# Optimization experiments

Hardware: AMD Instinct MI355X
Metric: run time of the kernel (lower is better)

Reference implementation:

```python
import jax, jax.numpy as jnp
import numpy as np
import math

B, S, DM, H = 2, 2048, 1024, 16
HD = DM // H  # head_dim = 64


def setup_inputs() -> dict:
    key = jax.random.key(0)
    ks = jax.random.split(key, 7)
    mk = lambda k, shp, s=1.0: jax.random.normal(k, shp, dtype=jnp.float32) * s
    return {
        "q": mk(ks[0], (B, S, DM)),
        "k": mk(ks[1], (B, S, DM)),
        "v": mk(ks[2], (B, S, DM)),
        "wq": mk(ks[3], (DM, DM), 0.02),
        "wk": mk(ks[4], (DM, DM), 0.02),
        "wv": mk(ks[5], (DM, DM), 0.02),
        "wo": mk(ks[6], (DM, DM), 0.02),
    }


def reference(q, k, v, wq, wk, wv, wo):
    bsz, seqlen, _ = q.shape
    # bias-free linear projections: y = x @ W.T (torch nn.Linear layout [out,in])
    def proj(x, w):
        y = jnp.einsum('bsd,ed->bse', x, w)
        return y.reshape(bsz, seqlen, H, HD).transpose(0, 2, 1, 3)  # (B,H,S,HD)
    xq, xk, xv = proj(q, wq), proj(k, wk), proj(v, wv)
    scores = jnp.einsum('bhqd,bhkd->bhqk', xq, xk) / math.sqrt(HD)  # (B,H,S,S)
    # causal mask: -inf above the diagonal
    causal = jnp.tril(jnp.ones((seqlen, seqlen), dtype=bool))
    scores = jnp.where(causal[None, None], scores, -jnp.inf)
    probs = jax.nn.softmax(scores.astype(jnp.float32), axis=-1).astype(xq.dtype)
    # dropout p=0.0 -> identity in eval / p=0 config
    out = jnp.einsum('bhqk,bhkd->bhqd', probs, xv)  # (B,H,S,HD)
    out = out.transpose(0, 2, 1, 3).reshape(bsz, seqlen, DM)
    return jnp.einsum('bsd,ed->bse', out, wo)
```

## Files before the change

### kernel.cpp

```cpp
#include <hip/hip_runtime.h>
#include <hip/hip_bf16.h>
#include <stdint.h>

#define NB 2
#define NS 2048
#define NDM 1024
#define NH 16
#define NHD 64
#define NTOK (NB * NS)

typedef __bf16 bf16x8 __attribute__((ext_vector_type(8)));
typedef float f32x4 __attribute__((ext_vector_type(4)));
typedef uint16_t u16x8 __attribute__((ext_vector_type(8)));

static __device__ __forceinline__ uint16_t f2bf(float f) {
  __bf16 b = (__bf16)f;
  union { __bf16 b; uint16_t u; } x; x.b = b;
  return x.u;
}

static __device__ __forceinline__ u16x8 cvt8(float4 a, float4 b) {
  u16x8 v;
  v[0] = f2bf(a.x); v[1] = f2bf(a.y); v[2] = f2bf(a.z); v[3] = f2bf(a.w);
  v[4] = f2bf(b.x); v[5] = f2bf(b.y); v[6] = f2bf(b.z); v[7] = f2bf(b.w);
  return v;
}

static __device__ __forceinline__ void gload_lds16(const void* g, void* l) {
  __builtin_amdgcn_global_load_lds(
      (const __attribute__((address_space(1))) void*)g,
      (__attribute__((address_space(3))) void*)l, 16, 0, 0);
}

__global__ __launch_bounds__(256) void cvt_all(
    const float* __restrict__ wq, const float* __restrict__ wk,
    const float* __restrict__ wv, const float* __restrict__ wo,
    const float* __restrict__ q, const float* __restrict__ k,
    const float* __restrict__ v, uint16_t* __restrict__ WQB,
    uint16_t* __restrict__ WKB, uint16_t* __restrict__ WVB,
    uint16_t* __restrict__ WOB, uint16_t* __restrict__ XBQ,
    uint16_t* __restrict__ XBK, uint16_t* __restrict__ XBV) {
  size_t E = ((size_t)blockIdx.x * 256 + threadIdx.x) * 8;
  const float* src;
  uint16_t* dst;
  size_t off;
  if (E < (size_t)(4u << 20)) {
    int s = (int)(E >> 20);
    off = E & ((1u << 20) - 1);
    src = (s == 0) ? wq : (s == 1) ? wk : (s == 2) ? wv : wo;
    dst = (s == 0) ? WQB : (s == 1) ? WKB : (s == 2) ? WVB : WOB;
  } else {
    size_t E2 = E - ((size_t)4u << 20);
    int s = (int)(E2 >> 22);
    off = E2 & ((1u << 22) - 1);
    src = (s == 0) ? q : (s == 1) ? k : v;
    dst = (s == 0) ? XBQ : (s == 1) ? XBK : XBV;
  }
  float4 a = *(const float4*)(src + off);
  float4 b = *(const float4*)(src + off + 4);
  *(u16x8*)&dst[off] = cvt8(a, b);
}

__global__ __launch_bounds__(256) void proj_gemm(
    const uint16_t* __restrict__ xbq, const uint16_t* __restrict__ xbk,
    const uint16_t* __restrict__ xbv, const uint16_t* __restrict__ wqb,
    const uint16_t* __restrict__ wkb, const uint16_t* __restrict__ wvb,
    uint16_t* __restrict__ XQ, uint16_t* __restrict__ XK,
    uint16_t* __restrict__ XVT) {
  __shared__ uint16_t SM[2][2][128][64];
  int z = blockIdx.z;
  const uint16_t* A = (z == 0) ? xbq : (z == 1) ? xbk : xbv;
  const uint16_t* W = (z == 0) ? wqb : (z == 1) ? wkb : wvb;
  int m0 = blockIdx.x * 128, n0 = blockIdx.y * 128;
  int tid = threadIdx.x;
  int lane = tid & 63, w = tid >> 6;
  int g = lane >> 4, r16 = lane & 15;
  int wm = w >> 1, wn = w & 1;
  int bce = ((lane & 7) ^ ((lane >> 3) & 7)) * 8;
  int brlane = lane >> 3;

  f32x4 acc[4][4] = {};

  #pragma unroll
  for (int i = 0; i < 4; ++i) {
    int row = w * 32 + i * 8;
    gload_lds16(A + (size_t)(m0 + row + brlane) * NDM + bce, &SM[0][0][row][0]);
    gload_lds16(W + (size_t)(n0 + row + brlane) * NDM + bce, &SM[0][1][row][0]);
  }
  __syncthreads();

  for (int t = 0; t < 16; ++t) {
    int cur = t & 1, nxt = cur ^ 1;
    if (t < 15) {
      int k1 = (t + 1) * 64;
      #pragma unroll
      for (int i = 0; i < 4; ++i) {
        int row = w * 32 + i * 8;
        gload_lds16(A + (size_t)(m0 + row + brlane) * NDM + k1 + bce,
                    &SM[nxt][0][row][0]);
        gload_lds16(W + (size_t)(n0 + row + brlane) * NDM + k1 + bce,
                    &SM[nxt][1][row][0]);
      }
    }

    #pragma unroll
    for (int kc = 0; kc < 2; ++kc) {
      bf16x8 af[4], bf[4];
      #pragma unroll
      for (int i = 0; i < 4; ++i) {
        int gran = (kc * 4 + g) ^ (r16 & 7);
        af[i] = *(const bf16x8*)&SM[cur][0][wm * 64 + i * 16 + r16][gran * 8];
        bf[i] = *(const bf16x8*)&SM[cur][1][wn * 64 + i * 16 + r16][gran * 8];
      }
      #pragma unroll
      for (int mi = 0; mi < 4; ++mi)
        #pragma unroll
        for (int ni = 0; ni < 4; ++ni)
          acc[mi][ni] = __builtin_amdgcn_mfma_f32_16x16x32_bf16(
              af[mi], bf[ni], acc[mi][ni], 0, 0, 0);
    }
    __syncthreads();
  }

  if (z == 2) {
    uint16_t* T = &SM[0][0][0][0];
    #pragma unroll
    for (int mi = 0; mi < 4; ++mi) {
      #pragma unroll
      for (int ni = 0; ni < 4; ++ni) {
        int tr = wn * 64 + ni * 16 + r16;
        int tc = wm * 64 + mi * 16 + g * 4;
        int gran = tc >> 3, sub = g & 1;
        f32x4 a = acc[mi][ni];
        ushort4 pk;
        pk.x = f2bf(a[0]); pk.y = f2bf(a[1]);
        pk.z = f2bf(a[2]); pk.w = f2bf(a[3]);
        *(ushort4*)(T + tr * 128 + ((gran ^ (tr & 7)) << 3) + (sub << 2)) = pk;
      }
    }
    __syncthreads();
    #pragma unroll
    for (int it = 0; it < 8; ++it) {
      int row = it * 16 + (tid >> 4);
      int grn = tid & 15;
      u16x8 vv = *(const u16x8*)(T + row * 128 + ((grn ^ (row & 7)) << 3));
      *(u16x8*)&XVT[(size_t)(n0 + row) * NTOK + m0 + grn * 8] = vv;
    }
  } else {
    float scale = (z == 0) ? 0.125f * 1.44269504088896340736f : 1.0f;
    uint16_t* Y = (z == 0) ? XQ : XK;
    #pragma unroll
    for (int mi = 0; mi < 4; ++mi) {
      #pragma unroll
      for (int ni = 0; ni < 4; ++ni) {
        int m = m0 + wm * 64 + mi * 16 + g * 4;
        int n = n0 + wn * 64 + ni * 16 + r16;
        f32x4 a = acc[mi][ni];
        #pragma unroll
        for (int j = 0; j < 4; ++j)
          Y[(size_t)(m + j) * NDM + n] = f2bf(a[j] * scale);
      }
    }
  }
}

__global__ __launch_bounds__(256) void attn_kernel(
    const uint16_t* __restrict__ XQ, const uint16_t* __restrict__ XK,
    const uint16_t* __restrict__ XVT, uint16_t* __restrict__ AO) {
  __shared__ uint16_t Klds[2][64][72];
  __shared__ uint16_t Vlds[2][64][72];
  __shared__ uint16_t Plds[4][16][72];

  int tid = threadIdx.x;
  int lane = tid & 63;
  int w = tid >> 6;
  int g = lane >> 4, r16 = lane & 15;
  int srow = tid >> 2;
  int scol = (tid & 3) * 16;

  int item = (int)blockIdx.x;
  int qc = 31 - (item >> 5);
  int bh = item & 31;
  int b = bh >> 4, h = bh & 15;
  int q0 = qc * 64;
  int q0w = q0 + w * 16;
  int T = qc + 1;

  const uint16_t* qb =
      XQ + (size_t)(b * NS + q0w + r16) * NDM + h * NHD + g * 8;
  bf16x8 qf0 = *(const bf16x8*)qb;
  bf16x8 qf1 = *(const bf16x8*)(qb + 32);

  f32x4 oacc[4] = {};
  float mrow = -1e30f, lsum = 0.f;

  const uint16_t* kbase = XK + (size_t)(b * NS + srow) * NDM + h * NHD + scol;
  const uint16_t* vbase = XVT + (size_t)(h * NHD + srow) * NTOK + b * NS + scol;

  u16x8 kr0 = *(const u16x8*)(kbase);
  u16x8 kr1 = *(const u16x8*)(kbase + 8);
  u16x8 vr0 = *(const u16x8*)(vbase);
  u16x8 vr1 = *(const u16x8*)(vbase + 8);

  for (int t = 0; t < T; ++t) {
    int kv0 = t * 64;
    int cur = t & 1;
    *(u16x8*)&Klds[cur][srow][scol]     = kr0;
    *(u16x8*)&Klds[cur][srow][scol + 8] = kr1;
    *(u16x8*)&Vlds[cur][srow][scol]     = vr0;
    *(u16x8*)&Vlds[cur][srow][scol + 8] = vr1;
    __syncthreads();
    if (t + 1 < T) {
      const uint16_t* kp = kbase + (size_t)(t + 1) * 64 * NDM;
      const uint16_t* vp = vbase + (t + 1) * 64;
      kr0 = *(const u16x8*)(kp);
      kr1 = *(const u16x8*)(kp + 8);
      vr0 = *(const u16x8*)(vp);
      vr1 = *(const u16x8*)(vp + 8);
    }

    f32x4 sc[4];
    __builtin_amdgcn_s_setprio(1);
    #pragma unroll
    for (int t4 = 0; t4 < 4; ++t4) {
      bf16x8 kf0 = *(const bf16x8*)&Klds[cur][t4 * 16 + r16][g * 8];
      bf16x8 kf1 = *(const bf16x8*)&Klds[cur][t4 * 16 + r16][32 + g * 8];
      f32x4 x = __builtin_amdgcn_mfma_f32_16x16x32_bf16(
          kf0, qf0, (f32x4){0.f, 0.f, 0.f, 0.f}, 0, 0, 0);
      x = __builtin_amdgcn_mfma_f32_16x16x32_bf16(kf1, qf1, x, 0, 0, 0);
      sc[t4] = x;
    }
    __builtin_amdgcn_s_setprio(0);

    #pragma unroll
    for (int t4 = 0; t4 < 4; ++t4) {
      if (kv0 + t4 * 16 + 15 > q0w) {
        #pragma unroll
        for (int j = 0; j < 4; ++j)
          if (kv0 + t4 * 16 + g * 4 + j > q0w + r16) sc[t4][j] = -1e30f;
      }
    }

    float m16 = fmaxf(
        fmaxf(fmaxf(fmaxf(sc[0][0], sc[0][1]), fmaxf(sc[0][2], sc[0][3])),
              fmaxf(fmaxf(sc[1][0], sc[1][1]), fmaxf(sc[1][2], sc[1][3]))),
        fmaxf(fmaxf(fmaxf(sc[2][0], sc[2][1]), fmaxf(sc[2][2], sc[2][3])),
              fmaxf(fmaxf(sc[3][0], sc[3][1]), fmaxf(sc[3][2], sc[3][3]))));
    m16 = fmaxf(m16, __shfl_xor(m16, 16));
    m16 = fmaxf(m16, __shfl_xor(m16, 32));

    if (!__all(m16 <= mrow + 8.0f)) {
      float mnew = fmaxf(mrow, m16);
      float sf = __builtin_amdgcn_exp2f(mrow - mnew);
      mrow = mnew;
      lsum *= sf;
      #pragma unroll
      for (int j = 0; j < 4; ++j) {
        float sfj = __shfl(sf, g * 4 + j);
        #pragma unroll
        for (int dt = 0; dt < 4; ++dt) oacc[dt][j] *= sfj;
      }
    }

    #pragma unroll
    for (int t4 = 0; t4 < 4; ++t4) {
      float p0 = __builtin_amdgcn_exp2f(sc[t4][0] - mrow);
      float p1 = __builtin_amdgcn_exp2f(sc[t4][1] - mrow);
      float p2 = __builtin_amdgcn_exp2f(sc[t4][2] - mrow);
      float p3 = __builtin_amdgcn_exp2f(sc[t4][3] - mrow);
      lsum += (p0 + p1) + (p2 + p3);
      ushort4 pk;
      pk.x = f2bf(p0); pk.y = f2bf(p1); pk.z = f2bf(p2); pk.w = f2bf(p3);
      *(ushort4*)&Plds[w][r16][t4 * 16 + g * 4] = pk;
    }

    bf16x8 pa0 = *(const bf16x8*)&Plds[w][r16][g * 8];
    bf16x8 pa1 = *(const bf16x8*)&Plds[w][r16][32 + g * 8];
    __builtin_amdgcn_s_setprio(1);
    #pragma unroll
    for (int dt = 0; dt < 4; ++dt) {
      bf16x8 vf0 = *(const bf16x8*)&Vlds[cur][dt * 16 + r16][g * 8];
      bf16x8 vf1 = *(const bf16x8*)&Vlds[cur][dt * 16 + r16][32 + g * 8];
      oacc[dt] = __builtin_amdgcn_mfma_f32_16x16x32_bf16(pa0, vf0, oacc[dt], 0, 0, 0);
      oacc[dt] = __builtin_amdgcn_mfma_f32_16x16x32_bf16(pa1, vf1, oacc[dt], 0, 0, 0);
    }
    __builtin_amdgcn_s_setprio(0);
  }

  float l2 = lsum + __shfl_xor(lsum, 16);
  float ltot = l2 + __shfl_xor(l2, 32);
  #pragma unroll
  for (int j = 0; j < 4; ++j) {
    float lt = __shfl(ltot, g * 4 + j);
    float inv = 1.0f / lt;
    size_t ro = (size_t)(b * NS + q0 + w * 16 + g * 4 + j) * NDM + h * NHD;
    #pragma unroll
    for (int dt = 0; dt < 4; ++dt)
      AO[ro + dt * 16 + r16] = f2bf(oacc[dt][j] * inv);
  }
}

__global__ __launch_bounds__(256) void out_gemm(
    const uint16_t* __restrict__ AO, const uint16_t* __restrict__ wob,
    float* __restrict__ out) {
  __shared__ uint16_t As[2][128][64];
  __shared__ uint16_t Bs[2][128][64];
  int m0 = blockIdx.x * 128, n0 = blockIdx.y * 128;
  int tid = threadIdx.x;
  int lane = tid & 63, w = tid >> 6;
  int g = lane >> 4, r16 = lane & 15;
  int wm = w >> 1, wn = w & 1;
  int bce = ((lane & 7) ^ ((lane >> 3) & 7)) * 8;
  int brlane = lane >> 3;

  f32x4 acc[4][4] = {};

  #pragma unroll
  for (int i = 0; i < 4; ++i) {
    int row = w * 32 + i * 8;
    gload_lds16(AO + (size_t)(m0 + row + brlane) * NDM + bce, &As[0][row][0]);
    gload_lds16(wob + (size_t)(n0 + row + brlane) * NDM + bce, &Bs[0][row][0]);
  }
  __syncthreads();

  for (int t = 0; t < 16; ++t) {
    int cur = t & 1, nxt = cur ^ 1;
    if (t < 15) {
      int k1 = (t + 1) * 64;
      #pragma unroll
      for (int i = 0; i < 4; ++i) {
        int row = w * 32 + i * 8;
        gload_lds16(AO + (size_t)(m0 + row + brlane) * NDM + k1 + bce,
                    &As[nxt][row][0]);
        gload_lds16(wob + (size_t)(n0 + row + brlane) * NDM + k1 + bce,
                    &Bs[nxt][row][0]);
      }
    }

    #pragma unroll
    for (int kc = 0; kc < 2; ++kc) {
      bf16x8 af[4], bf[4];
      #pragma unroll
      for (int i = 0; i < 4; ++i) {
        int gran = (kc * 4 + g) ^ (r16 & 7);
        af[i] = *(const bf16x8*)&As[cur][wm * 64 + i * 16 + r16][gran * 8];
        bf[i] = *(const bf16x8*)&Bs[cur][wn * 64 + i * 16 + r16][gran * 8];
      }
      #pragma unroll
      for (int mi = 0; mi < 4; ++mi)
        #pragma unroll
        for (int ni = 0; ni < 4; ++ni)
          acc[mi][ni] = __builtin_amdgcn_mfma_f32_16x16x32_bf16(
              af[mi], bf[ni], acc[mi][ni], 0, 0, 0);
    }
    __syncthreads();
  }

  #pragma unroll
  for (int mi = 0; mi < 4; ++mi) {
    #pragma unroll
    for (int ni = 0; ni < 4; ++ni) {
      int m = m0 + wm * 64 + mi * 16 + g * 4;
      int n = n0 + wn * 64 + ni * 16 + r16;
      #pragma unroll
      for (int j = 0; j < 4; ++j)
        out[(size_t)(m + j) * NDM + n] = acc[mi][ni][j];
    }
  }
}

extern "C" void kernel_launch(void* const* d_in, const int* in_sizes, int n_in,
                              void* d_out, int out_size, void* d_ws,
                              size_t ws_size, hipStream_t stream) {
  const float* q  = (const float*)d_in[0];
  const float* k  = (const float*)d_in[1];
  const float* v  = (const float*)d_in[2];
  const float* wq = (const float*)d_in[3];
  const float* wk = (const float*)d_in[4];
  const float* wv = (const float*)d_in[5];
  const float* wo = (const float*)d_in[6];

  const size_t XN = (size_t)NTOK * NDM;
  const size_t WN = (size_t)NDM * NDM;
  uint16_t* XQ  = (uint16_t*)d_ws;
  uint16_t* XK  = XQ + XN;
  uint16_t* XVT = XK + XN;
  uint16_t* WQB = XVT + XN;
  uint16_t* WKB = WQB + WN;
  uint16_t* WVB = WKB + WN;
  uint16_t* WOB = WVB + WN;
  uint16_t* XBQ = WOB + WN;
  uint16_t* XBK = XBQ + XN;
  uint16_t* XBV = XBK + XN;
  uint16_t* AO  = XBQ;

  cvt_all<<<dim3(8192), 256, 0, stream>>>(
      wq, wk, wv, wo, q, k, v, WQB, WKB, WVB, WOB, XBQ, XBK, XBV);
  proj_gemm<<<dim3(NTOK / 128, NDM / 128, 3), 256, 0, stream>>>(
      XBQ, XBK, XBV, WQB, WKB, WVB, XQ, XK, XVT);
  attn_kernel<<<dim3(1024), 256, 0, stream>>>(XQ, XK, XVT, AO);
  out_gemm<<<dim3(NTOK / 128, NDM / 128), 256, 0, stream>>>(
      AO, WOB, (float*)d_out);
}
```

Measured before the change: 110.8 us.

## Rewrite attention kernel with 32x32 MFMA, in-register P, and async LDS loads

```diff
diff --git a/kernel.cpp b/kernel.cpp
--- a/kernel.cpp
+++ b/kernel.cpp
@@ -11,6 +11,7 @@
 
 typedef __bf16 bf16x8 __attribute__((ext_vector_type(8)));
 typedef float f32x4 __attribute__((ext_vector_type(4)));
+typedef float f32x16 __attribute__((ext_vector_type(16)));
 typedef uint16_t u16x8 __attribute__((ext_vector_type(8)));
 
 static __device__ __forceinline__ uint16_t f2bf(float f) {
@@ -30,6 +31,16 @@
   __builtin_amdgcn_global_load_lds(
       (const __attribute__((address_space(1))) void*)g,
       (__attribute__((address_space(3))) void*)l, 16, 0, 0);
+}
+
+static __device__ __forceinline__ int cvtpk(float lo, float hi) {
+  int r;
+  asm("v_cvt_pk_bf16_f32 %0, %1, %2" : "=v"(r) : "v"(lo), "v"(hi));
+  return r;
+}
+
+static __device__ __forceinline__ void pl32swap(int& a, int& b) {
+  asm volatile("v_permlane32_swap_b32 %0, %1" : "+v"(a), "+v"(b));
 }
 
 __global__ __launch_bounds__(256) void cvt_all(
@@ -164,139 +175,151 @@
   }
 }
 
-__global__ __launch_bounds__(256) void attn_kernel(
+__global__ __launch_bounds__(128) void attn_kernel(
     const uint16_t* __restrict__ XQ, const uint16_t* __restrict__ XK,
     const uint16_t* __restrict__ XVT, uint16_t* __restrict__ AO) {
-  __shared__ uint16_t Klds[2][64][72];
-  __shared__ uint16_t Vlds[2][64][72];
-  __shared__ uint16_t Plds[4][16][72];
+  __shared__ uint16_t Klds[2][64][64];
+  __shared__ uint16_t Vlds[2][64][64];
 
   int tid = threadIdx.x;
   int lane = tid & 63;
   int w = tid >> 6;
-  int g = lane >> 4, r16 = lane & 15;
-  int srow = tid >> 2;
-  int scol = (tid & 3) * 16;
+  int q32 = lane & 31;
+  int hi = lane >> 5;
+  int l7 = lane & 7;
 
   int item = (int)blockIdx.x;
   int qc = 31 - (item >> 5);
   int bh = item & 31;
   int b = bh >> 4, h = bh & 15;
   int q0 = qc * 64;
-  int q0w = q0 + w * 16;
+  int q0w = q0 + w * 32;
   int T = qc + 1;
 
-  const uint16_t* qb =
-      XQ + (size_t)(b * NS + q0w + r16) * NDM + h * NHD + g * 8;
-  bf16x8 qf0 = *(const bf16x8*)qb;
-  bf16x8 qf1 = *(const bf16x8*)(qb + 32);
-
-  f32x4 oacc[4] = {};
+  bf16x8 qf[4];
+  const uint16_t* qrow =
+      XQ + (size_t)(b * NS + q0w + q32) * NDM + h * NHD + hi * 8;
+  #pragma unroll
+  for (int dc = 0; dc < 4; ++dc) qf[dc] = *(const bf16x8*)(qrow + dc * 16);
+
+  f32x16 oacc[2] = {};
   float mrow = -1e30f, lsum = 0.f;
 
-  const uint16_t* kbase = XK + (size_t)(b * NS + srow) * NDM + h * NHD + scol;
-  const uint16_t* vbase = XVT + (size_t)(h * NHD + srow) * NTOK + b * NS + scol;
-
-  u16x8 kr0 = *(const u16x8*)(kbase);
-  u16x8 kr1 = *(const u16x8*)(kbase + 8);
-  u16x8 vr0 = *(const u16x8*)(vbase);
-  u16x8 vr1 = *(const u16x8*)(vbase + 8);
+  int srl = lane >> 3;
+  int bce = (l7 ^ srl) * 8;
+  const uint16_t* kstg = XK + (size_t)(b * NS + srl) * NDM + h * NHD + bce;
+  const uint16_t* vstg = XVT + (size_t)(h * NHD + srl) * NTOK + b * NS + bce;
+
+  #pragma unroll
+  for (int i = 0; i < 4; ++i) {
+    int base = i * 16 + w * 8;
+    gload_lds16(kstg + (size_t)base * NDM, &Klds[0][base][0]);
+    gload_lds16(vstg + (size_t)base * NTOK, &Vlds[0][base][0]);
+  }
 
   for (int t = 0; t < T; ++t) {
     int kv0 = t * 64;
     int cur = t & 1;
-    *(u16x8*)&Klds[cur][srow][scol]     = kr0;
-    *(u16x8*)&Klds[cur][srow][scol + 8] = kr1;
-    *(u16x8*)&Vlds[cur][srow][scol]     = vr0;
-    *(u16x8*)&Vlds[cur][srow][scol + 8] = vr1;
     __syncthreads();
     if (t + 1 < T) {
-      const uint16_t* kp = kbase + (size_t)(t + 1) * 64 * NDM;
-      const uint16_t* vp = vbase + (t + 1) * 64;
-      kr0 = *(const u16x8*)(kp);
-      kr1 = *(const u16x8*)(kp + 8);
-      vr0 = *(const u16x8*)(vp);
-      vr1 = *(const u16x8*)(vp + 8);
-    }
-
-    f32x4 sc[4];
-    __builtin_amdgcn_s_setprio(1);
-    #pragma unroll
-    for (int t4 = 0; t4 < 4; ++t4) {
-      bf16x8 kf0 = *(const bf16x8*)&Klds[cur][t4 * 16 + r16][g * 8];
-      bf16x8 kf1 = *(const bf16x8*)&Klds[cur][t4 * 16 + r16][32 + g * 8];
-      f32x4 x = __builtin_amdgcn_mfma_f32_16x16x32_bf16(
-          kf0, qf0, (f32x4){0.f, 0.f, 0.f, 0.f}, 0, 0, 0);
-      x = __builtin_amdgcn_mfma_f32_16x16x32_bf16(kf1, qf1, x, 0, 0, 0);
-      sc[t4] = x;
-    }
-    __builtin_amdgcn_s_setprio(0);
-
-    #pragma unroll
-    for (int t4 = 0; t4 < 4; ++t4) {
-      if (kv0 + t4 * 16 + 15 > q0w) {
+      int kv1 = kv0 + 64;
+      #pragma unroll
+      for (int i = 0; i < 4; ++i) {
+        int base = i * 16 + w * 8;
+        gload_lds16(kstg + (size_t)(kv1 + base) * NDM, &Klds[cur ^ 1][base][0]);
+        gload_lds16(vstg + kv1 + (size_t)base * NTOK, &Vlds[cur ^ 1][base][0]);
+      }
+    }
+
+    #pragma unroll
+    for (int sb = 0; sb < 2; ++sb) {
+      int kvb0 = kv0 + sb * 32;
+      if (kvb0 > q0w + 31) continue;
+
+      f32x16 sacc = {};
+      __builtin_amdgcn_s_setprio(1);
+      #pragma unroll
+      for (int dc = 0; dc < 4; ++dc) {
+        bf16x8 kf = *(const bf16x8*)
+            &Klds[cur][sb * 32 + q32][(((dc << 1) + hi) ^ l7) * 8];
+        sacc = __builtin_amdgcn_mfma_f32_32x32x16_bf16(kf, qf[dc], sacc, 0, 0, 0);
+      }
+      __builtin_amdgcn_s_setprio(0);
+
+      if (kvb0 + 31 > q0w) {
+        int qg = q0w + q32;
         #pragma unroll
-        for (int j = 0; j < 4; ++j)
-          if (kv0 + t4 * 16 + g * 4 + j > q0w + r16) sc[t4][j] = -1e30f;
-      }
-    }
-
-    float m16 = fmaxf(
-        fmaxf(fmaxf(fmaxf(sc[0][0], sc[0][1]), fmaxf(sc[0][2], sc[0][3])),
-              fmaxf(fmaxf(sc[1][0], sc[1][1]), fmaxf(sc[1][2], sc[1][3]))),
-        fmaxf(fmaxf(fmaxf(sc[2][0], sc[2][1]), fmaxf(sc[2][2], sc[2][3])),
-              fmaxf(fmaxf(sc[3][0], sc[3][1]), fmaxf(sc[3][2], sc[3][3]))));
-    m16 = fmaxf(m16, __shfl_xor(m16, 16));
-    m16 = fmaxf(m16, __shfl_xor(m16, 32));
-
-    if (!__all(m16 <= mrow + 8.0f)) {
-      float mnew = fmaxf(mrow, m16);
-      float sf = __builtin_amdgcn_exp2f(mrow - mnew);
-      mrow = mnew;
-      lsum *= sf;
-      #pragma unroll
-      for (int j = 0; j < 4; ++j) {
-        float sfj = __shfl(sf, g * 4 + j);
+        for (int r = 0; r < 16; ++r) {
+          int kv = kvb0 + (r & 3) + 8 * (r >> 2) + 4 * hi;
+          if (kv > qg) sacc[r] = -1e30f;
+        }
+      }
+
+      float ma = fmaxf(fmaxf(sacc[0], sacc[1]), fmaxf(sacc[2], sacc[3]));
+      float mb = fmaxf(fmaxf(sacc[4], sacc[5]), fmaxf(sacc[6], sacc[7]));
+      float mc = fmaxf(fmaxf(sacc[8], sacc[9]), fmaxf(sacc[10], sacc[11]));
+      float md = fmaxf(fmaxf(sacc[12], sacc[13]), fmaxf(sacc[14], sacc[15]));
+      float m16 = fmaxf(fmaxf(ma, mb), fmaxf(mc, md));
+      m16 = fmaxf(m16, __shfl_xor(m16, 32));
+
+      if (!__all(m16 <= mrow + 8.0f)) {
+        float mnew = fmaxf(mrow, m16);
+        float sf = __builtin_amdgcn_exp2f(mrow - mnew);
+        mrow = mnew;
+        lsum *= sf;
+        oacc[0] *= sf;
+        oacc[1] *= sf;
+      }
+
+      float p[16];
+      float ls = 0.f;
+      #pragma unroll
+      for (int r = 0; r < 16; ++r) {
+        p[r] = __builtin_amdgcn_exp2f(sacc[r] - mrow);
+        ls += p[r];
+      }
+      lsum += ls;
+
+      #pragma unroll
+      for (int kvb = 0; kvb < 2; ++kvb) {
+        int base = kvb * 8;
+        int A0 = cvtpk(p[base + 0], p[base + 1]);
+        int A1 = cvtpk(p[base + 2], p[base + 3]);
+        int B0 = cvtpk(p[base + 4], p[base + 5]);
+        int B1 = cvtpk(p[base + 6], p[base + 7]);
+        pl32swap(A0, B0);
+        pl32swap(A1, B1);
+        union { int wds[4]; bf16x8 f; } pf;
+        pf.wds[0] = A0; pf.wds[1] = A1; pf.wds[2] = B0; pf.wds[3] = B1;
+
+        __builtin_amdgcn_s_setprio(1);
         #pragma unroll
-        for (int dt = 0; dt < 4; ++dt) oacc[dt][j] *= sfj;
-      }
-    }
-
-    #pragma unroll
-    for (int t4 = 0; t4 < 4; ++t4) {
-      float p0 = __builtin_amdgcn_exp2f(sc[t4][0] - mrow);
-      float p1 = __builtin_amdgcn_exp2f(sc[t4][1] - mrow);
-      float p2 = __builtin_amdgcn_exp2f(sc[t4][2] - mrow);
-      float p3 = __builtin_amdgcn_exp2f(sc[t4][3] - mrow);
-      lsum += (p0 + p1) + (p2 + p3);
+        for (int dh = 0; dh < 2; ++dh) {
+          bf16x8 vf = *(const bf16x8*)
+              &Vlds[cur][dh * 32 + q32]
+                   [((sb * 4 + (kvb << 1) + hi) ^ l7) * 8];
+          oacc[dh] = __builtin_amdgcn_mfma_f32_32x32x16_bf16(
+              vf, pf.f, oacc[dh], 0, 0, 0);
+        }
+        __builtin_amdgcn_s_setprio(0);
+      }
+    }
+  }
+
+  float ltot = lsum + __shfl_xor(lsum, 32);
+  float inv = 1.0f / ltot;
+  size_t ro = (size_t)(b * NS + q0w + q32) * NDM + h * NHD;
+  #pragma unroll
+  for (int dh = 0; dh < 2; ++dh) {
+    #pragma unroll
+    for (int rq = 0; rq < 4; ++rq) {
       ushort4 pk;
-      pk.x = f2bf(p0); pk.y = f2bf(p1); pk.z = f2bf(p2); pk.w = f2bf(p3);
-      *(ushort4*)&Plds[w][r16][t4 * 16 + g * 4] = pk;
-    }
-
-    bf16x8 pa0 = *(const bf16x8*)&Plds[w][r16][g * 8];
-    bf16x8 pa1 = *(const bf16x8*)&Plds[w][r16][32 + g * 8];
-    __builtin_amdgcn_s_setprio(1);
-    #pragma unroll
-    for (int dt = 0; dt < 4; ++dt) {
-      bf16x8 vf0 = *(const bf16x8*)&Vlds[cur][dt * 16 + r16][g * 8];
-      bf16x8 vf1 = *(const bf16x8*)&Vlds[cur][dt * 16 + r16][32 + g * 8];
-      oacc[dt] = __builtin_amdgcn_mfma_f32_16x16x32_bf16(pa0, vf0, oacc[dt], 0, 0, 0);
-      oacc[dt] = __builtin_amdgcn_mfma_f32_16x16x32_bf16(pa1, vf1, oacc[dt], 0, 0, 0);
-    }
-    __builtin_amdgcn_s_setprio(0);
-  }
-
-  float l2 = lsum + __shfl_xor(lsum, 16);
-  float ltot = l2 + __shfl_xor(l2, 32);
-  #pragma unroll
-  for (int j = 0; j < 4; ++j) {
-    float lt = __shfl(ltot, g * 4 + j);
-    float inv = 1.0f / lt;
-    size_t ro = (size_t)(b * NS + q0 + w * 16 + g * 4 + j) * NDM + h * NHD;
-    #pragma unroll
-    for (int dt = 0; dt < 4; ++dt)
-      AO[ro + dt * 16 + r16] = f2bf(oacc[dt][j] * inv);
+      pk.x = f2bf(oacc[dh][rq * 4 + 0] * inv);
+      pk.y = f2bf(oacc[dh][rq * 4 + 1] * inv);
+      pk.z = f2bf(oacc[dh][rq * 4 + 2] * inv);
+      pk.w = f2bf(oacc[dh][rq * 4 + 3] * inv);
+      *(ushort4*)&AO[ro + dh * 32 + rq * 8 + hi * 4] = pk;
+    }
   }
 }
 
@@ -398,7 +421,7 @@
       wq, wk, wv, wo, q, k, v, WQB, WKB, WVB, WOB, XBQ, XBK, XBV);
   proj_gemm<<<dim3(NTOK / 128, NDM / 128, 3), 256, 0, stream>>>(
       XBQ, XBK, XBV, WQB, WKB, WVB, XQ, XK, XVT);
-  attn_kernel<<<dim3(1024), 256, 0, stream>>>(XQ, XK, XVT, AO);
+  attn_kernel<<<dim3(1024), 128, 0, stream>>>(XQ, XK, XVT, AO);
   out_gemm<<<dim3(NTOK / 128, NDM / 128), 256, 0, stream>>>(
       AO, WOB, (float*)d_out);
 }
```

New measurement: 133.7 us. 20.7% more time.

## Stage K/V tiles with direct global-to-LDS loads and XOR-swizzled layout

Applied to the files above, without the earlier changes.

```diff
diff --git a/kernel.cpp b/kernel.cpp
--- a/kernel.cpp
+++ b/kernel.cpp
@@ -167,16 +167,15 @@
 __global__ __launch_bounds__(256) void attn_kernel(
     const uint16_t* __restrict__ XQ, const uint16_t* __restrict__ XK,
     const uint16_t* __restrict__ XVT, uint16_t* __restrict__ AO) {
-  __shared__ uint16_t Klds[2][64][72];
-  __shared__ uint16_t Vlds[2][64][72];
+  __shared__ uint16_t Klds[2][64][64];
+  __shared__ uint16_t Vlds[2][64][64];
   __shared__ uint16_t Plds[4][16][72];
 
   int tid = threadIdx.x;
   int lane = tid & 63;
   int w = tid >> 6;
   int g = lane >> 4, r16 = lane & 15;
-  int srow = tid >> 2;
-  int scol = (tid & 3) * 16;
+  int swz = r16 & 7;
 
   int item = (int)blockIdx.x;
   int qc = 31 - (item >> 5);
@@ -194,37 +193,49 @@
   f32x4 oacc[4] = {};
   float mrow = -1e30f, lsum = 0.f;
 
-  const uint16_t* kbase = XK + (size_t)(b * NS + srow) * NDM + h * NHD + scol;
-  const uint16_t* vbase = XVT + (size_t)(h * NHD + srow) * NTOK + b * NS + scol;
-
-  u16x8 kr0 = *(const u16x8*)(kbase);
-  u16x8 kr1 = *(const u16x8*)(kbase + 8);
-  u16x8 vr0 = *(const u16x8*)(vbase);
-  u16x8 vr1 = *(const u16x8*)(vbase + 8);
+  int srl = lane >> 3;
+  int bce = ((lane & 7) ^ srl) * 8;
+  const uint16_t* kstg = XK + (size_t)(b * NS + srl) * NDM + h * NHD + bce;
+  const uint16_t* vstg = XVT + (size_t)(h * NHD + srl) * NTOK + b * NS + bce;
+  int stgrow = (w & 1) * 32;
+
+  if (w < 2) {
+    #pragma unroll
+    for (int i = 0; i < 4; ++i)
+      gload_lds16(kstg + (size_t)(stgrow + i * 8) * NDM,
+                  &Klds[0][stgrow + i * 8][0]);
+  } else {
+    #pragma unroll
+    for (int i = 0; i < 4; ++i)
+      gload_lds16(vstg + (size_t)(stgrow + i * 8) * NTOK,
+                  &Vlds[0][stgrow + i * 8][0]);
+  }
 
   for (int t = 0; t < T; ++t) {
     int kv0 = t * 64;
     int cur = t & 1;
-    *(u16x8*)&Klds[cur][srow][scol]     = kr0;
-    *(u16x8*)&Klds[cur][srow][scol + 8] = kr1;
-    *(u16x8*)&Vlds[cur][srow][scol]     = vr0;
-    *(u16x8*)&Vlds[cur][srow][scol + 8] = vr1;
     __syncthreads();
     if (t + 1 < T) {
-      const uint16_t* kp = kbase + (size_t)(t + 1) * 64 * NDM;
-      const uint16_t* vp = vbase + (t + 1) * 64;
-      kr0 = *(const u16x8*)(kp);
-      kr1 = *(const u16x8*)(kp + 8);
-      vr0 = *(const u16x8*)(vp);
-      vr1 = *(const u16x8*)(vp + 8);
+      int kv1 = kv0 + 64;
+      if (w < 2) {
+        #pragma unroll
+        for (int i = 0; i < 4; ++i)
+          gload_lds16(kstg + (size_t)(kv1 + stgrow + i * 8) * NDM,
+                      &Klds[cur ^ 1][stgrow + i * 8][0]);
+      } else {
+        #pragma unroll
+        for (int i = 0; i < 4; ++i)
+          gload_lds16(vstg + kv1 + (size_t)(stgrow + i * 8) * NTOK,
+                      &Vlds[cur ^ 1][stgrow + i * 8][0]);
+      }
     }
 
     f32x4 sc[4];
     __builtin_amdgcn_s_setprio(1);
     #pragma unroll
     for (int t4 = 0; t4 < 4; ++t4) {
-      bf16x8 kf0 = *(const bf16x8*)&Klds[cur][t4 * 16 + r16][g * 8];
-      bf16x8 kf1 = *(const bf16x8*)&Klds[cur][t4 * 16 + r16][32 + g * 8];
+      bf16x8 kf0 = *(const bf16x8*)&Klds[cur][t4 * 16 + r16][(g ^ swz) * 8];
+      bf16x8 kf1 = *(const bf16x8*)&Klds[cur][t4 * 16 + r16][((4 + g) ^ swz) * 8];
       f32x4 x = __builtin_amdgcn_mfma_f32_16x16x32_bf16(
           kf0, qf0, (f32x4){0.f, 0.f, 0.f, 0.f}, 0, 0, 0);
       x = __builtin_amdgcn_mfma_f32_16x16x32_bf16(kf1, qf1, x, 0, 0, 0);
@@ -279,8 +290,8 @@
     __builtin_amdgcn_s_setprio(1);
     #pragma unroll
     for (int dt = 0; dt < 4; ++dt) {
-      bf16x8 vf0 = *(const bf16x8*)&Vlds[cur][dt * 16 + r16][g * 8];
-      bf16x8 vf1 = *(const bf16x8*)&Vlds[cur][dt * 16 + r16][32 + g * 8];
+      bf16x8 vf0 = *(const bf16x8*)&Vlds[cur][dt * 16 + r16][(g ^ swz) * 8];
+      bf16x8 vf1 = *(const bf16x8*)&Vlds[cur][dt * 16 + r16][((4 + g) ^ swz) * 8];
       oacc[dt] = __builtin_amdgcn_mfma_f32_16x16x32_bf16(pa0, vf0, oacc[dt], 0, 0, 0);
       oacc[dt] = __builtin_amdgcn_mfma_f32_16x16x32_bf16(pa1, vf1, oacc[dt], 0, 0, 0);
     }
```

After: 110.3 us (median of 2 runs). About the same (-0.4%).
